# Kernel optimization log

Measured on AMD Instinct MI355X. Metric: run time of the kernel, lower is better.

Reference implementation:

```python
import jax, jax.numpy as jnp
import numpy as np

IN_FT = 256
OUT_FT = 256


def setup_inputs() -> dict:
    key = jax.random.key(0)
    k1, k2, k3 = jax.random.split(key, 3)
    B, N = 4, 4096
    seq = jax.random.normal(k1, (B, N, IN_FT), dtype=jnp.float32)
    adj = jax.random.uniform(k2, (B, N, N), dtype=jnp.float32)
    # Xavier-uniform fc weight [out_ft, in_ft], bias zeros
    limit = float(np.sqrt(6.0 / (IN_FT + OUT_FT)))
    W = jax.random.uniform(k3, (OUT_FT, IN_FT), minval=-limit, maxval=limit, dtype=jnp.float32)
    b = jnp.zeros((OUT_FT,), dtype=jnp.float32)
    alpha = jnp.array(0.25, dtype=jnp.float32)  # PReLU shared parameter
    return {"seq": seq, "adj": adj, "W": W, "b": b, "alpha": alpha}


def reference(seq, adj, W, b, alpha):
    # Linear projection: [B, N, out_ft]
    h = jnp.einsum("bni,oi->bno", seq, W) + b
    # Neighbor aggregation (dense bmm path): [B, N, N] @ [B, N, out_ft]
    h = jnp.einsum("bnm,bmo->bno", adj, h)
    # PReLU with shared alpha
    return jnp.where(h > 0, h, alpha * h)
```

## Files before the change

### kernel.cpp

```cpp
#include <hip/hip_runtime.h>
#include <hip/hip_bf16.h>

#define NSEQ 4096
#define FT 256
#define BK 64
#define NT (NSEQ / BK)

typedef __attribute__((ext_vector_type(8))) short bf16x8;
typedef __attribute__((ext_vector_type(4))) float f32x4;

__device__ __forceinline__ ushort f2bf(float f) {
  __hip_bfloat16 h = __float2bfloat16(f);
  return *reinterpret_cast<const ushort*>(&h);
}

__device__ __forceinline__ int swz(int row, int byteInRow) {
  return row * 128 + (byteInRow ^ ((row & 7) << 4));
}

__device__ __forceinline__ void mma_step(const char* lAp, const char* lBp,
                                         int lane, int wm, int wn,
                                         f32x4 acc[2][4]) {
  const int r16 = lane & 15;
  const int g16 = (lane >> 4) * 16;
#pragma unroll
  for (int kk = 0; kk < 2; ++kk) {
    const int kb = kk * 64 + g16;
    bf16x8 a[2], b[4];
#pragma unroll
    for (int mi = 0; mi < 2; ++mi) {
      const int row = wm * 32 + mi * 16 + r16;
      a[mi] = *reinterpret_cast<const bf16x8*>(lAp + swz(row, kb));
    }
#pragma unroll
    for (int ni = 0; ni < 4; ++ni) {
      const int row = wn * 64 + ni * 16 + r16;
      b[ni] = *reinterpret_cast<const bf16x8*>(lBp + swz(row, kb));
    }
#pragma unroll
    for (int mi = 0; mi < 2; ++mi)
#pragma unroll
      for (int ni = 0; ni < 4; ++ni)
        acc[mi][ni] = __builtin_amdgcn_mfma_f32_16x16x32_bf16(a[mi], b[ni],
                                                             acc[mi][ni], 0, 0, 0);
  }
}

__global__ __launch_bounds__(512) void linear_kernel(
    const float* __restrict__ seq, const float* __restrict__ W,
    const float* __restrict__ bias, ushort* __restrict__ hT) {
  __shared__ __align__(16) ushort lA[2][64 * 64];
  __shared__ __align__(16) ushort lB[2][256 * 64];

  const int tid = threadIdx.x;
  const int lane = tid & 63;
  const int wid = tid >> 6;
  const int wm = wid >> 2, wn = wid & 3;
  const int m0 = blockIdx.x * 64;

  const int ar = tid >> 4, ac = tid & 15;

  f32x4 rA[2];
  f32x4 rB[8];

  auto gload = [&](int t) {
    const int k0 = t * BK;
#pragma unroll
    for (int p = 0; p < 2; ++p)
      rA[p] = *reinterpret_cast<const f32x4*>(
          seq + (size_t)(m0 + ar + p * 32) * FT + k0 + ac * 4);
#pragma unroll
    for (int p = 0; p < 8; ++p)
      rB[p] = *reinterpret_cast<const f32x4*>(
          W + (size_t)(ar + p * 32) * FT + k0 + ac * 4);
  };
  auto lwrite = [&](int buf) {
    char* lAp = (char*)lA[buf];
    char* lBp = (char*)lB[buf];
#pragma unroll
    for (int p = 0; p < 2; ++p) {
      ushort4 u = make_ushort4(f2bf(rA[p][0]), f2bf(rA[p][1]), f2bf(rA[p][2]), f2bf(rA[p][3]));
      *reinterpret_cast<ushort4*>(lAp + swz(ar + p * 32, ac * 8)) = u;
    }
#pragma unroll
    for (int p = 0; p < 8; ++p) {
      ushort4 u = make_ushort4(f2bf(rB[p][0]), f2bf(rB[p][1]), f2bf(rB[p][2]), f2bf(rB[p][3]));
      *reinterpret_cast<ushort4*>(lBp + swz(ar + p * 32, ac * 8)) = u;
    }
  };

  f32x4 acc[2][4];
  const f32x4 zero = {0.f, 0.f, 0.f, 0.f};
#pragma unroll
  for (int mi = 0; mi < 2; ++mi)
#pragma unroll
    for (int ni = 0; ni < 4; ++ni) acc[mi][ni] = zero;

  gload(0);
  lwrite(0);
  const int NTA = FT / BK;
  for (int t = 0; t < NTA; ++t) {
    const int cur = t & 1;
    __syncthreads();
    if (t + 1 < NTA) gload(t + 1);
    mma_step((const char*)lA[cur], (const char*)lB[cur], lane, wm, wn, acc);
    if (t + 1 < NTA) lwrite(cur ^ 1);
  }

#pragma unroll
  for (int mi = 0; mi < 2; ++mi) {
    const int grow = m0 + wm * 32 + mi * 16 + ((lane >> 4) << 2);
    const int batch = grow >> 12;
    const int n = grow & (NSEQ - 1);
#pragma unroll
    for (int ni = 0; ni < 4; ++ni) {
      const int o = wn * 64 + ni * 16 + (lane & 15);
      const float bo = bias[o];
      ushort4 u;
      u.x = f2bf(acc[mi][ni][0] + bo);
      u.y = f2bf(acc[mi][ni][1] + bo);
      u.z = f2bf(acc[mi][ni][2] + bo);
      u.w = f2bf(acc[mi][ni][3] + bo);
      *reinterpret_cast<ushort4*>(hT + (size_t)(batch * FT + o) * NSEQ + n) = u;
    }
  }
}

__global__ __launch_bounds__(512) void bmm_prelu_kernel(
    const float* __restrict__ adj, const ushort* __restrict__ hT,
    const float* __restrict__ alphaP, float* __restrict__ out) {
  __shared__ __align__(16) ushort lA[2][64 * 64];
  __shared__ __align__(16) ushort lB[4][256 * 64];

  const int tid = threadIdx.x;
  const int lane = tid & 63;
  const int wid = tid >> 6;
  const int wm = wid >> 2, wn = wid & 3;

  const int bid = blockIdx.x;
  const int sbid = (bid & 7) * 32 + (bid >> 3);
  const int batch = sbid >> 6;
  const int m0 = (sbid & 63) * 64;

  const float* adjB = adj + (size_t)batch * NSEQ * NSEQ + (size_t)m0 * NSEQ;
  const ushort* hTB = hT + (size_t)batch * FT * NSEQ;

  const int ar = tid >> 4, ac = tid & 15;
  const int brow = wid * 8 + (lane >> 3);
  const int bg = (lane & 7) ^ (lane >> 3);

  f32x4 rA0[2], rA1[2];

  f32x4 acc[2][4];
  const f32x4 zero = {0.f, 0.f, 0.f, 0.f};
#pragma unroll
  for (int mi = 0; mi < 2; ++mi)
#pragma unroll
    for (int ni = 0; ni < 4; ++ni) acc[mi][ni] = zero;

  auto issueA = [&](int t, f32x4* r) {
    const int k0 = t * BK;
#pragma unroll
    for (int p = 0; p < 2; ++p)
      r[p] = __builtin_nontemporal_load(reinterpret_cast<const f32x4*>(
          adjB + (size_t)(ar + p * 32) * NSEQ + k0 + ac * 4));
  };
  auto issueB = [&](int t, int ib) {
    const int k0 = t * BK;
#pragma unroll
    for (int p = 0; p < 4; ++p) {
      const ushort* gp = hTB + (size_t)(p * 64 + brow) * NSEQ + k0 + bg * 8;
      ushort* lp = &lB[ib][p * 4096 + wid * 512];
      __builtin_amdgcn_global_load_lds(
          (const __attribute__((address_space(1))) void*)gp,
          (__attribute__((address_space(3))) void*)lp, 16, 0, 0);
    }
  };
  auto writeA = [&](const f32x4* r, int ia) {
    char* lAp = (char*)lA[ia];
#pragma unroll
    for (int p = 0; p < 2; ++p) {
      ushort4 u = make_ushort4(f2bf(r[p][0]), f2bf(r[p][1]), f2bf(r[p][2]), f2bf(r[p][3]));
      *reinterpret_cast<ushort4*>(lAp + swz(ar + p * 32, ac * 8)) = u;
    }
  };

  issueA(0, rA0);
  issueB(0, 0);
  issueB(1, 1);
  issueA(1, rA1);
  issueB(2, 2);
  asm volatile("s_waitcnt vmcnt(14)" ::: "memory");
  writeA(rA0, 0);
  asm volatile("s_waitcnt vmcnt(10) lgkmcnt(0)" ::: "memory");
  __builtin_amdgcn_s_barrier();
  __builtin_amdgcn_sched_barrier(0);

  auto body = [&](int t, f32x4* rIssue, f32x4* rWrite,
                  int ibIssue, int ibRead, int iaRead, int iaWrite) {
    issueA(t + 2, rIssue);
    issueB(t + 3, ibIssue);
    mma_step((const char*)lA[iaRead], (const char*)lB[ibRead], lane, wm, wn, acc);
    asm volatile("s_waitcnt vmcnt(10)" ::: "memory");
    writeA(rWrite, iaWrite);
    asm volatile("s_waitcnt lgkmcnt(0)" ::: "memory");
    __builtin_amdgcn_s_barrier();
    __builtin_amdgcn_sched_barrier(0);
  };

  for (int j = 0; j < 15; ++j) {
    body(j * 4 + 0, rA0, rA1, 3, 0, 0, 1);
    body(j * 4 + 1, rA1, rA0, 0, 1, 1, 0);
    body(j * 4 + 2, rA0, rA1, 1, 2, 0, 1);
    body(j * 4 + 3, rA1, rA0, 2, 3, 1, 0);
  }
  body(60, rA0, rA1, 3, 0, 0, 1);
  {
    issueA(63, rA1);
    mma_step((const char*)lA[1], (const char*)lB[1], lane, wm, wn, acc);
    asm volatile("s_waitcnt vmcnt(6)" ::: "memory");
    writeA(rA0, 0);
    asm volatile("s_waitcnt lgkmcnt(0)" ::: "memory");
    __builtin_amdgcn_s_barrier();
    __builtin_amdgcn_sched_barrier(0);
  }
  {
    mma_step((const char*)lA[0], (const char*)lB[2], lane, wm, wn, acc);
    asm volatile("s_waitcnt vmcnt(0)" ::: "memory");
    writeA(rA1, 1);
    asm volatile("s_waitcnt lgkmcnt(0)" ::: "memory");
    __builtin_amdgcn_s_barrier();
    __builtin_amdgcn_sched_barrier(0);
  }
  mma_step((const char*)lA[1], (const char*)lB[3], lane, wm, wn, acc);

  const float alpha = *alphaP;
  __syncthreads();
  float* lo = (float*)&lB[0][0];
  const int PITCH = 264;
#pragma unroll
  for (int mi = 0; mi < 2; ++mi) {
    const int rbase = wm * 32 + mi * 16 + ((lane >> 4) << 2);
#pragma unroll
    for (int ni = 0; ni < 4; ++ni) {
      const int o = wn * 64 + ni * 16 + (lane & 15);
#pragma unroll
      for (int j = 0; j < 4; ++j) {
        float v = acc[mi][ni][j];
        v = v > 0.f ? v : alpha * v;
        lo[(rbase + j) * PITCH + o] = v;
      }
    }
  }
  __syncthreads();
  float* outB = out + ((size_t)batch * NSEQ + m0) * FT;
  const int r = tid >> 3, c8 = tid & 7;
#pragma unroll
  for (int k = 0; k < 8; ++k) {
    const int g = c8 + k * 8;
    f32x4 v = *reinterpret_cast<const f32x4*>(lo + r * PITCH + g * 4);
    __builtin_nontemporal_store(v, reinterpret_cast<f32x4*>(outB + (size_t)r * FT + g * 4));
  }
}

extern "C" void kernel_launch(void* const* d_in, const int* in_sizes, int n_in,
                              void* d_out, int out_size, void* d_ws, size_t ws_size,
                              hipStream_t stream) {
  const float* seq = (const float*)d_in[0];
  const float* adj = (const float*)d_in[1];
  const float* W = (const float*)d_in[2];
  const float* bias = (const float*)d_in[3];
  const float* alpha = (const float*)d_in[4];
  float* out = (float*)d_out;
  ushort* hT = (ushort*)d_ws;

  linear_kernel<<<256, 512, 0, stream>>>(seq, W, bias, hT);
  bmm_prelu_kernel<<<256, 512, 0, stream>>>(adj, hT, alpha, out);
}
```

Before: 93.59 us.

## Halve bmm tile to 32 rows and 32-deep K, doubling grid for occupancy

Reworks the adjacency-times-features kernel to use 32-row output tiles and a 32-wide K step instead of 64x64. Each of the 8 waves now owns a 32-column slice of the output. The launch now has 512 blocks and a launch-bounds hint of 4 blocks per SM. A-tile prefetch is deepened to three stages with 2-float loads, and B keeps a 4-stage LDS ring. The aim is more resident blocks and better latency hiding on the bandwidth-bound adj stream, at the cost of reading hT twice as often and paying more barriers per unit of work.

Result: slower. 153.6 us (+64.1%).

```diff
diff --git a/kernel.cpp b/kernel.cpp
--- a/kernel.cpp
+++ b/kernel.cpp
@@ -4,10 +4,10 @@
 #define NSEQ 4096
 #define FT 256
 #define BK 64
-#define NT (NSEQ / BK)
 
 typedef __attribute__((ext_vector_type(8))) short bf16x8;
 typedef __attribute__((ext_vector_type(4))) float f32x4;
+typedef __attribute__((ext_vector_type(2))) float f32x2;
 
 __device__ __forceinline__ ushort f2bf(float f) {
   __hip_bfloat16 h = __float2bfloat16(f);
@@ -126,124 +126,140 @@
   }
 }
 
-__global__ __launch_bounds__(512) void bmm_prelu_kernel(
+#define BKB 32
+#define NTB (NSEQ / BKB)
+
+__global__ __launch_bounds__(512, 4) void bmm_prelu_kernel(
     const float* __restrict__ adj, const ushort* __restrict__ hT,
     const float* __restrict__ alphaP, float* __restrict__ out) {
-  __shared__ __align__(16) ushort lA[2][64 * 64];
-  __shared__ __align__(16) ushort lB[4][256 * 64];
+  __shared__ __align__(16) char smem[4 * 16384 + 2 * 2048];
 
   const int tid = threadIdx.x;
   const int lane = tid & 63;
   const int wid = tid >> 6;
-  const int wm = wid >> 2, wn = wid & 3;
 
   const int bid = blockIdx.x;
-  const int sbid = (bid & 7) * 32 + (bid >> 3);
-  const int batch = sbid >> 6;
-  const int m0 = (sbid & 63) * 64;
+  const int sbid = (bid & 7) * 64 + (bid >> 3);
+  const int batch = sbid >> 7;
+  const int m0 = (sbid & 127) * 32;
 
   const float* adjB = adj + (size_t)batch * NSEQ * NSEQ + (size_t)m0 * NSEQ;
   const ushort* hTB = hT + (size_t)batch * FT * NSEQ;
 
   const int ar = tid >> 4, ac = tid & 15;
-  const int brow = wid * 8 + (lane >> 3);
-  const int bg = (lane & 7) ^ (lane >> 3);
-
-  f32x4 rA0[2], rA1[2];
-
-  f32x4 acc[2][4];
+  const int brow = wid * 16 + (lane >> 2);
+  const int bgsrc = (lane & 3) ^ ((lane >> 2) & 3);
+
+  f32x2 rA0, rA1, rA2, rA3;
+
+  f32x4 acc[2][2];
   const f32x4 zero = {0.f, 0.f, 0.f, 0.f};
 #pragma unroll
   for (int mi = 0; mi < 2; ++mi)
 #pragma unroll
-    for (int ni = 0; ni < 4; ++ni) acc[mi][ni] = zero;
-
-  auto issueA = [&](int t, f32x4* r) {
-    const int k0 = t * BK;
-#pragma unroll
-    for (int p = 0; p < 2; ++p)
-      r[p] = __builtin_nontemporal_load(reinterpret_cast<const f32x4*>(
-          adjB + (size_t)(ar + p * 32) * NSEQ + k0 + ac * 4));
+    for (int ni = 0; ni < 2; ++ni) acc[mi][ni] = zero;
+
+  auto issueA = [&](int t, f32x2& r) {
+    r = __builtin_nontemporal_load(reinterpret_cast<const f32x2*>(
+        adjB + (size_t)ar * NSEQ + t * BKB + ac * 2));
   };
   auto issueB = [&](int t, int ib) {
-    const int k0 = t * BK;
-#pragma unroll
-    for (int p = 0; p < 4; ++p) {
-      const ushort* gp = hTB + (size_t)(p * 64 + brow) * NSEQ + k0 + bg * 8;
-      ushort* lp = &lB[ib][p * 4096 + wid * 512];
+    const int k0 = t * BKB;
+#pragma unroll
+    for (int p = 0; p < 2; ++p) {
+      const ushort* gp = hTB + (size_t)(p * 128 + brow) * NSEQ + k0 + bgsrc * 8;
+      char* lp = smem + ib * 16384 + p * 8192 + wid * 1024;
       __builtin_amdgcn_global_load_lds(
           (const __attribute__((address_space(1))) void*)gp,
           (__attribute__((address_space(3))) void*)lp, 16, 0, 0);
     }
   };
-  auto writeA = [&](const f32x4* r, int ia) {
-    char* lAp = (char*)lA[ia];
-#pragma unroll
-    for (int p = 0; p < 2; ++p) {
-      ushort4 u = make_ushort4(f2bf(r[p][0]), f2bf(r[p][1]), f2bf(r[p][2]), f2bf(r[p][3]));
-      *reinterpret_cast<ushort4*>(lAp + swz(ar + p * 32, ac * 8)) = u;
-    }
-  };
-
-  issueA(0, rA0);
-  issueB(0, 0);
-  issueB(1, 1);
-  issueA(1, rA1);
-  issueB(2, 2);
-  asm volatile("s_waitcnt vmcnt(14)" ::: "memory");
+  auto writeA = [&](const f32x2& r, int ia) {
+    char* lAp = smem + 65536 + ia * 2048;
+    uint pack = (uint)f2bf(r[0]) | ((uint)f2bf(r[1]) << 16);
+    *reinterpret_cast<uint*>(lAp + ar * 64 + ((ac * 4) ^ ((ar & 3) << 4))) = pack;
+  };
+  auto mma = [&](int ia, int ib) {
+    const char* lAp = smem + 65536 + ia * 2048;
+    const char* lBp = smem + ib * 16384;
+    const int r16 = lane & 15;
+    const int gofs = ((lane >> 4) ^ (lane & 3)) << 4;
+    bf16x8 a[2], b[2];
+#pragma unroll
+    for (int mi = 0; mi < 2; ++mi)
+      a[mi] = *reinterpret_cast<const bf16x8*>(lAp + (mi * 16 + r16) * 64 + gofs);
+#pragma unroll
+    for (int ni = 0; ni < 2; ++ni)
+      b[ni] = *reinterpret_cast<const bf16x8*>(
+          lBp + (wid * 32 + ni * 16 + r16) * 64 + gofs);
+#pragma unroll
+    for (int mi = 0; mi < 2; ++mi)
+#pragma unroll
+      for (int ni = 0; ni < 2; ++ni)
+        acc[mi][ni] = __builtin_amdgcn_mfma_f32_16x16x32_bf16(a[mi], b[ni],
+                                                             acc[mi][ni], 0, 0, 0);
+  };
+
+  issueA(0, rA0); __builtin_amdgcn_sched_barrier(0);
+  issueB(0, 0);   __builtin_amdgcn_sched_barrier(0);
+  issueA(1, rA1); __builtin_amdgcn_sched_barrier(0);
+  issueB(1, 1);   __builtin_amdgcn_sched_barrier(0);
+  issueA(2, rA2); __builtin_amdgcn_sched_barrier(0);
+  issueB(2, 2);   __builtin_amdgcn_sched_barrier(0);
+  asm volatile("s_waitcnt vmcnt(8)" ::: "memory");
   writeA(rA0, 0);
-  asm volatile("s_waitcnt vmcnt(10) lgkmcnt(0)" ::: "memory");
+  asm volatile("s_waitcnt vmcnt(6) lgkmcnt(0)" ::: "memory");
   __builtin_amdgcn_s_barrier();
   __builtin_amdgcn_sched_barrier(0);
 
-  auto body = [&](int t, f32x4* rIssue, f32x4* rWrite,
-                  int ibIssue, int ibRead, int iaRead, int iaWrite) {
-    issueA(t + 2, rIssue);
-    issueB(t + 3, ibIssue);
-    mma_step((const char*)lA[iaRead], (const char*)lB[ibRead], lane, wm, wn, acc);
-    asm volatile("s_waitcnt vmcnt(10)" ::: "memory");
-    writeA(rWrite, iaWrite);
+  auto body = [&](int t, f32x2& rIss, const f32x2& rWr,
+                  int ibIss, int ibRd, int iaRd, int iaWr) {
+    issueA(t + 3, rIss);
+    issueB(t + 3, ibIss);
+    mma(iaRd, ibRd);
+    asm volatile("s_waitcnt vmcnt(6)" ::: "memory");
+    writeA(rWr, iaWr);
     asm volatile("s_waitcnt lgkmcnt(0)" ::: "memory");
     __builtin_amdgcn_s_barrier();
     __builtin_amdgcn_sched_barrier(0);
   };
 
-  for (int j = 0; j < 15; ++j) {
-    body(j * 4 + 0, rA0, rA1, 3, 0, 0, 1);
-    body(j * 4 + 1, rA1, rA0, 0, 1, 1, 0);
-    body(j * 4 + 2, rA0, rA1, 1, 2, 0, 1);
-    body(j * 4 + 3, rA1, rA0, 2, 3, 1, 0);
-  }
-  body(60, rA0, rA1, 3, 0, 0, 1);
+  for (int j = 0; j < 31; ++j) {
+    const int t0 = j * 4;
+    body(t0 + 0, rA3, rA1, 3, 0, 0, 1);
+    body(t0 + 1, rA0, rA2, 0, 1, 1, 0);
+    body(t0 + 2, rA1, rA3, 1, 2, 0, 1);
+    body(t0 + 3, rA2, rA0, 2, 3, 1, 0);
+  }
+  body(124, rA3, rA1, 3, 0, 0, 1);
   {
-    issueA(63, rA1);
-    mma_step((const char*)lA[1], (const char*)lB[1], lane, wm, wn, acc);
-    asm volatile("s_waitcnt vmcnt(6)" ::: "memory");
-    writeA(rA0, 0);
+    mma(1, 1);
+    asm volatile("s_waitcnt vmcnt(3)" ::: "memory");
+    writeA(rA2, 0);
     asm volatile("s_waitcnt lgkmcnt(0)" ::: "memory");
     __builtin_amdgcn_s_barrier();
     __builtin_amdgcn_sched_barrier(0);
   }
   {
-    mma_step((const char*)lA[0], (const char*)lB[2], lane, wm, wn, acc);
+    mma(0, 2);
     asm volatile("s_waitcnt vmcnt(0)" ::: "memory");
-    writeA(rA1, 1);
+    writeA(rA3, 1);
     asm volatile("s_waitcnt lgkmcnt(0)" ::: "memory");
     __builtin_amdgcn_s_barrier();
     __builtin_amdgcn_sched_barrier(0);
   }
-  mma_step((const char*)lA[1], (const char*)lB[3], lane, wm, wn, acc);
+  mma(1, 3);
 
   const float alpha = *alphaP;
   __syncthreads();
-  float* lo = (float*)&lB[0][0];
+  float* lo = (float*)smem;
   const int PITCH = 264;
 #pragma unroll
   for (int mi = 0; mi < 2; ++mi) {
-    const int rbase = wm * 32 + mi * 16 + ((lane >> 4) << 2);
-#pragma unroll
-    for (int ni = 0; ni < 4; ++ni) {
-      const int o = wn * 64 + ni * 16 + (lane & 15);
+    const int rbase = mi * 16 + ((lane >> 4) << 2);
+#pragma unroll
+    for (int ni = 0; ni < 2; ++ni) {
+      const int o = wid * 32 + ni * 16 + (lane & 15);
 #pragma unroll
       for (int j = 0; j < 4; ++j) {
         float v = acc[mi][ni][j];
@@ -254,10 +270,10 @@
   }
   __syncthreads();
   float* outB = out + ((size_t)batch * NSEQ + m0) * FT;
-  const int r = tid >> 3, c8 = tid & 7;
-#pragma unroll
-  for (int k = 0; k < 8; ++k) {
-    const int g = c8 + k * 8;
+  const int r = tid >> 4, c16 = tid & 15;
+#pragma unroll
+  for (int k = 0; k < 4; ++k) {
+    const int g = c16 + k * 16;
     f32x4 v = *reinterpret_cast<const f32x4*>(lo + r * PITCH + g * 4);
     __builtin_nontemporal_store(v, reinterpret_cast<f32x4*>(outB + (size_t)r * FT + g * 4));
   }
@@ -275,5 +291,5 @@
   ushort* hT = (ushort*)d_ws;
 
   linear_kernel<<<256, 512, 0, stream>>>(seq, W, bias, hT);
-  bmm_prelu_kernel<<<256, 512, 0, stream>>>(adj, hT, alpha, out);
-}
+  bmm_prelu_kernel<<<512, 512, 0, stream>>>(adj, hT, alpha, out);
+}
```

## Deepen adj register prefetch to three stages and raise MFMA priority

Applied to the files above, without the earlier changes.

Adds two more register buffers for the fp32 adj tiles so global loads are issued three tiles ahead instead of two, with vmcnt waits and buffer rotation adjusted to match. The adj loads become ordinary cached loads instead of nontemporal ones. The MFMA step is wrapped in s_setprio to favour the compute wave over others. This aims to hide more of the HBM latency on the dominant adj stream, at the cost of extra VGPRs and a more fragile waitcnt bookkeeping.

Measured after the change: 90.51 us. 1.03x faster.

```diff
diff --git a/kernel.cpp b/kernel.cpp
--- a/kernel.cpp
+++ b/kernel.cpp
@@ -149,7 +149,7 @@
   const int brow = wid * 8 + (lane >> 3);
   const int bg = (lane & 7) ^ (lane >> 3);
 
-  f32x4 rA0[2], rA1[2];
+  f32x4 rA0[2], rA1[2], rA2[2], rA3[2];
 
   f32x4 acc[2][4];
   const f32x4 zero = {0.f, 0.f, 0.f, 0.f};
@@ -162,8 +162,8 @@
     const int k0 = t * BK;
 #pragma unroll
     for (int p = 0; p < 2; ++p)
-      r[p] = __builtin_nontemporal_load(reinterpret_cast<const f32x4*>(
-          adjB + (size_t)(ar + p * 32) * NSEQ + k0 + ac * 4));
+      r[p] = *reinterpret_cast<const f32x4*>(
+          adjB + (size_t)(ar + p * 32) * NSEQ + k0 + ac * 4);
   };
   auto issueB = [&](int t, int ib) {
     const int k0 = t * BK;
@@ -187,47 +187,53 @@
 
   issueA(0, rA0);
   issueB(0, 0);
+  issueA(1, rA1);
   issueB(1, 1);
-  issueA(1, rA1);
+  issueA(2, rA2);
   issueB(2, 2);
-  asm volatile("s_waitcnt vmcnt(14)" ::: "memory");
+  asm volatile("s_waitcnt vmcnt(16)" ::: "memory");
   writeA(rA0, 0);
-  asm volatile("s_waitcnt vmcnt(10) lgkmcnt(0)" ::: "memory");
+  asm volatile("s_waitcnt vmcnt(12) lgkmcnt(0)" ::: "memory");
   __builtin_amdgcn_s_barrier();
   __builtin_amdgcn_sched_barrier(0);
 
-  auto body = [&](int t, f32x4* rIssue, f32x4* rWrite,
-                  int ibIssue, int ibRead, int iaRead, int iaWrite) {
-    issueA(t + 2, rIssue);
-    issueB(t + 3, ibIssue);
-    mma_step((const char*)lA[iaRead], (const char*)lB[ibRead], lane, wm, wn, acc);
-    asm volatile("s_waitcnt vmcnt(10)" ::: "memory");
-    writeA(rWrite, iaWrite);
+  auto body = [&](int t, f32x4* rIss, const f32x4* rWr,
+                  int ibIss, int ibRd, int iaRd, int iaWr) {
+    issueA(t + 3, rIss);
+    issueB(t + 3, ibIss);
+    __builtin_amdgcn_s_setprio(1);
+    mma_step((const char*)lA[iaRd], (const char*)lB[ibRd], lane, wm, wn, acc);
+    __builtin_amdgcn_s_setprio(0);
+    asm volatile("s_waitcnt vmcnt(12)" ::: "memory");
+    writeA(rWr, iaWr);
     asm volatile("s_waitcnt lgkmcnt(0)" ::: "memory");
     __builtin_amdgcn_s_barrier();
     __builtin_amdgcn_sched_barrier(0);
   };
 
   for (int j = 0; j < 15; ++j) {
-    body(j * 4 + 0, rA0, rA1, 3, 0, 0, 1);
-    body(j * 4 + 1, rA1, rA0, 0, 1, 1, 0);
-    body(j * 4 + 2, rA0, rA1, 1, 2, 0, 1);
-    body(j * 4 + 3, rA1, rA0, 2, 3, 1, 0);
-  }
-  body(60, rA0, rA1, 3, 0, 0, 1);
+    body(j * 4 + 0, rA3, rA1, 3, 0, 0, 1);
+    body(j * 4 + 1, rA0, rA2, 0, 1, 1, 0);
+    body(j * 4 + 2, rA1, rA3, 1, 2, 0, 1);
+    body(j * 4 + 3, rA2, rA0, 2, 3, 1, 0);
+  }
+  body(60, rA3, rA1, 3, 0, 0, 1);
   {
-    issueA(63, rA1);
+    __builtin_amdgcn_s_setprio(1);
     mma_step((const char*)lA[1], (const char*)lB[1], lane, wm, wn, acc);
+    __builtin_amdgcn_s_setprio(0);
     asm volatile("s_waitcnt vmcnt(6)" ::: "memory");
-    writeA(rA0, 0);
+    writeA(rA2, 0);
     asm volatile("s_waitcnt lgkmcnt(0)" ::: "memory");
     __builtin_amdgcn_s_barrier();
     __builtin_amdgcn_sched_barrier(0);
   }
   {
+    __builtin_amdgcn_s_setprio(1);
     mma_step((const char*)lA[0], (const char*)lB[2], lane, wm, wn, acc);
+    __builtin_amdgcn_s_setprio(0);
     asm volatile("s_waitcnt vmcnt(0)" ::: "memory");
-    writeA(rA1, 1);
+    writeA(rA3, 1);
     asm volatile("s_waitcnt lgkmcnt(0)" ::: "memory");
     __builtin_amdgcn_s_barrier();
     __builtin_amdgcn_sched_barrier(0);
```
